# Optimization experiments

Hardware: AMD Instinct MI355X
Metric: run time of the kernel (lower is better)

## Reference

```python
import jax, jax.numpy as jnp
import numpy as np

# SLAYER neuron / simulation parameters (from netParams)
THETA = 10.0      # spike threshold
TAU_SR = 10.0     # synaptic (psp) alpha-kernel time constant
TAU_REF = 1.0     # refractory alpha-kernel time constant
SCALE_REF = 2.0   # refractory kernel scale
TS = 1.0          # simulation time step

N, C, H, W_SP, T = 8, 2, 50, 63, 500
OUT = 128


def _alpha_scan(x_t_first, tau, gain):
    """Causal convolution with alpha kernel k[dt] = gain*(dt*TS/tau)*exp(1-dt*TS/tau),
    k[0]=0, expressed as an exact 2-state linear recursion (O(T) instead of O(T^2)).
    x_t_first: [T, ...]. Returns [T, ...]."""
    r = jnp.exp(jnp.asarray(-TS / tau, x_t_first.dtype))
    c = jnp.asarray(gain * (TS / tau) * np.e, x_t_first.dtype)

    def step(carry, xt):
        A, B = carry          # A = sum c*dt*r^dt, B = sum c*r^dt over past inputs
        out = A               # kernel is 0 at dt=0, so x[t] does not contribute yet
        Bp = B + c * xt
        return (r * (A + Bp), r * Bp), out

    zeros = jnp.zeros_like(x_t_first[0])
    _, out = jax.lax.scan(step, (zeros, zeros), x_t_first)
    return out


def _spike_scan(u_t_first):
    """SLAYER getSpikes: sequential threshold with refractory alpha kernel
    nu[dt] = -SCALE_REF*THETA*(dt*TS/TAU_REF)*exp(1-dt*TS/TAU_REF).
    u_t_first: [T, N, O] membrane input. Returns spikes [T, N, O]."""
    r = jnp.exp(jnp.asarray(-TS / TAU_REF, u_t_first.dtype))
    c = jnp.asarray(-SCALE_REF * THETA * (TS / TAU_REF) * np.e, u_t_first.dtype)

    def step(carry, ut):
        A, B = carry
        u = ut + A                       # membrane + accumulated refractory response
        s = (u >= THETA).astype(u.dtype)
        Bp = B + c * s
        return (r * (A + Bp), r * Bp), s

    zeros = jnp.zeros_like(u_t_first[0])
    _, s = jax.lax.scan(step, (zeros, zeros), u_t_first)
    return s


def setup_inputs() -> dict:
    key = jax.random.key(0)
    k1, k2 = jax.random.split(key)
    downsampled = (jax.random.uniform(k1, (N, C, H, W_SP, T)) < 0.05).astype(jnp.float32)
    W = jax.random.normal(k2, (OUT, C * H * W_SP), dtype=jnp.float32) * 0.05
    return {"downsampled": downsampled, "W": W}


def reference(downsampled, W):
    # psp: alpha-kernel temporal filter over every input element
    x = jnp.moveaxis(downsampled, -1, 0)            # [T, N, C, H, W]
    a = _alpha_scan(x, TAU_SR, 1.0)                  # [T, N, C, H, W]
    # dense: full-spatial projection per time step
    a = a.reshape(T, N, C * H * W_SP)                # [T, N, CHW]
    u = jnp.einsum('tnc,oc->tno', a, W)              # [T, N, OUT]
    # spike generation with refractory dynamics
    s = _spike_scan(u)                               # [T, N, OUT]
    s = jnp.moveaxis(s, 0, -1)                       # [N, OUT, T]
    return s.reshape(N, OUT, 1, 1, T)                # SLAYER dense output layout
```

## Files before the change

kernel.cpp:

```cpp
#include <hip/hip_runtime.h>

#define NB 8
#define CHW 6300
#define TT 500
#define OUT 128
#define NO 1024
#define NK32 200
#define KSPLIT 8
#define NKC (NK32/KSPLIT)

typedef __attribute__((ext_vector_type(8))) _Float16 f16x8;
typedef __attribute__((ext_vector_type(4))) float f32x4;

__global__ __launch_bounds__(512) void packW(const float* __restrict__ W,
                                             _Float16* __restrict__ Wp) {
    const int tid = threadIdx.x;
    const int of = tid >> 6;
    const int lane = tid & 63;
    const int k32 = blockIdx.x;
    const int hl = blockIdx.y;
    const int o = of * 16 + (lane & 15);
    const int cb = k32 * 32 + (lane >> 4) * 8;

    union { _Float16 h[8]; uint4 u; } tmp;
#pragma unroll
    for (int i = 0; i < 8; i++) {
        int c = cb + i;
        float w = (c < CHW) ? W[(size_t)o * CHW + c] : 0.f;
        _Float16 hi = (_Float16)w;
        tmp.h[i] = (hl == 0) ? hi : (_Float16)((w - (float)hi) * 2048.f);
    }
    size_t lr = (((size_t)hl * NK32 + k32) * 8 + of) * 64 + lane;
    *(uint4*)(Wp + lr * 8) = tmp.u;
}

__global__ __launch_bounds__(256, 2) void gemm(const float* __restrict__ x,
                                               const _Float16* __restrict__ Wp,
                                               float* __restrict__ vp) {
    const int L = blockIdx.x;
    const int ks = L & 7;
    const int n  = (L >> 3) & 7;
    const int tg = L >> 6;
    const int tid = threadIdx.x;
    const int w = tid >> 6;
    const int lane = tid & 63;
    const int l15 = lane & 15;
    const int lg = lane >> 4;
    const int t0 = (tg * 4 + w) * 16;
    const int k32_0 = ks * NKC;

    __shared__ float Xl[4][32][17];

    const float* xn = x + (size_t)n * CHW * TT;
    const int xr = lane >> 2;
    const int xc4 = (lane & 3) * 4;
    const bool t_ok = (t0 + xc4 + 4) <= TT;
    const float4 f4z = make_float4(0.f, 0.f, 0.f, 0.f);

    f32x4 acc[8][2] = {};
    f16x8 wA[16], wB[16];
    float4 q0[2], q1[2];

#define XG(qq, it_)                                                            \
    {                                                                          \
        _Pragma("unroll") for (int p_ = 0; p_ < 2; p_++) {                     \
            const int c_ = (k32_0 + (it_)) * 32 + xr + 16 * p_;                \
            qq[p_] = (c_ < CHW && t_ok)                                        \
                ? *(const float4*)(xn + (size_t)c_ * TT + t0 + xc4)            \
                : f4z;                                                         \
        }                                                                      \
    }

#define DSW(qq)                                                                \
    {                                                                          \
        _Pragma("unroll") for (int p_ = 0; p_ < 2; p_++) {                     \
            const int r_ = xr + 16 * p_;                                       \
            Xl[w][r_][xc4 + 0] = qq[p_].x;                                     \
            Xl[w][r_][xc4 + 1] = qq[p_].y;                                     \
            Xl[w][r_][xc4 + 2] = qq[p_].z;                                     \
            Xl[w][r_][xc4 + 3] = qq[p_].w;                                     \
        }                                                                      \
    }

#define TRANS(bfr_)                                                            \
    {                                                                          \
        union { _Float16 h[8]; f16x8 v; } tc_;                                 \
        _Pragma("unroll") for (int i_ = 0; i_ < 8; i_++)                       \
            tc_.h[i_] = (_Float16)Xl[w][lg * 8 + i_][l15];                     \
        bfr_ = tc_.v;                                                          \
    }

#define WRL(wd, it_)                                                           \
    _Pragma("unroll") for (int f_ = 0; f_ < 16; f_++) {                        \
        const int hl_ = f_ & 1, of_ = f_ >> 1;                                 \
        wd[f_] = *(const f16x8*)(Wp +                                          \
            ((((size_t)hl_ * NK32 + k32_0 + (it_)) * 8 + of_) * 64 + lane) * 8); \
    }

#define COMP(bfr_, wd)                                                         \
    _Pragma("unroll") for (int of_ = 0; of_ < 8; of_++)                        \
        _Pragma("unroll") for (int hl_ = 0; hl_ < 2; hl_++)                    \
            acc[of_][hl_] = __builtin_amdgcn_mfma_f32_16x16x32_f16(            \
                wd[of_ * 2 + hl_], bfr_, acc[of_][hl_], 0, 0, 0);

    WRL(wA, 0)
    XG(q0, 0)
    XG(q1, 1)
    DSW(q0)

    for (int p = 0; p < 12; ++p) {
        {
            const int s = 2 * p;
            WRL(wB, s + 1)
            XG(q0, s + 2)
            f16x8 bfr;
            TRANS(bfr)
            DSW(q1)
            COMP(bfr, wA)
        }
        {
            const int s = 2 * p + 1;
            WRL(wA, s + 1)
            if (p < 11) { XG(q1, s + 2) }
            f16x8 bfr;
            TRANS(bfr)
            DSW(q0)
            COMP(bfr, wB)
        }
    }
    {
        f16x8 bfr;
        TRANS(bfr)
        COMP(bfr, wA)
    }

    const float inv = 1.f / 2048.f;
    const int t = t0 + l15;
    if (t < TT) {
#pragma unroll
        for (int of = 0; of < 8; of++) {
            f32x4 vo;
#pragma unroll
            for (int r = 0; r < 4; r++)
                vo[r] = acc[of][0][r] + acc[of][1][r] * inv;
            *(f32x4*)(vp + (((size_t)ks * TT + t) * NB + n) * OUT +
                      of * 16 + lg * 4) = vo;
        }
    }
#undef XG
#undef DSW
#undef TRANS
#undef WRL
#undef COMP
}

#define SCN_RA 0.9048374180359595f
#define SCN_RACA 0.24596031111569496f
#define SCN_RS 0.36787944117144233f
#define SCN_RSCS -20.0f
#define SCN_RSCS2 -40.0f
#define SCN_RSRSCS -7.3575888234288467f
#define SCN_TH 10.0f

#define CHAIN_STEP(i)                                                   \
    {                                                                   \
        float ua = Aa;                                                  \
        float w = fmaf(SCN_RS, G, ua);                                  \
        float u = sp ? (w + SCN_RSCS) : w;                              \
        bool sn = (u >= SCN_TH);                                        \
        sbuf[i][lane] = sn ? 1.f : 0.f;                                 \
        float Gb = fmaf(SCN_RS, G, H);                                  \
        G = sp ? (Gb + SCN_RSCS2) : Gb;                                 \
        float Hb = SCN_RS * H;                                          \
        H = sp ? (Hb + SCN_RSRSCS) : Hb;                                \
        sp = sn;                                                        \
        Ba = fmaf(SCN_RA, Ba, SCN_RACA * vv[i]);                        \
        Aa = fmaf(SCN_RA, Aa, Ba);                                      \
    }

__global__ __launch_bounds__(512) void scanspike(const float* __restrict__ vp,
                                                 float* __restrict__ out) {
    const int tid = threadIdx.x;
    const int wave = tid >> 6;
    const int lane = tid & 63;
    const int l5 = lane & 31;
    const int rh = lane >> 5;
    const int g0 = blockIdx.x * 32;
    const int cn = g0 >> 7;
    const int co = (g0 & 127) + l5;

    __shared__ float vbuf[2][64][32];
    __shared__ float sbuf[64][33];

    for (int rp = wave; rp * 2 < 64; rp += 8) {
        int r = rp * 2 + rh;
        float a = 0.f;
#pragma unroll
        for (int k = 0; k < KSPLIT; k++)
            a += vp[(((size_t)k * TT + r) * NB + cn) * OUT + co];
        vbuf[0][r][l5] = a;
    }
    __syncthreads();

    float Aa = 0.f, Ba = 0.f, G = 0.f, H = 0.f;
    bool sp = false;

    for (int tb = 0; tb < 8; ++tb) {
        const int cur = tb & 1;
        const int t0 = tb * 64;
        const int cnt = (tb == 7) ? 52 : 64;

        if (wave == 0) {
            if (lane < 32) {
                if (cnt == 64) {
                    float vv[64];
#pragma unroll
                    for (int i = 0; i < 64; ++i) vv[i] = vbuf[cur][i][l5];
#pragma unroll
                    for (int i = 0; i < 64; ++i) CHAIN_STEP(i)
                } else {
                    float vv[52];
#pragma unroll
                    for (int i = 0; i < 52; ++i) vv[i] = vbuf[cur][i][l5];
#pragma unroll
                    for (int i = 0; i < 52; ++i) CHAIN_STEP(i)
                }
            }
        } else if (tb < 7) {
            const int nt0 = t0 + 64;
            const int ncnt = (tb == 6) ? 52 : 64;
            for (int rp = wave - 1; rp * 2 < ncnt; rp += 7) {
                int r = rp * 2 + rh;
                float a = 0.f;
#pragma unroll
                for (int k = 0; k < KSPLIT; k++)
                    a += vp[(((size_t)k * TT + nt0 + r) * NB + cn) * OUT + co];
                vbuf[cur ^ 1][r][l5] = a;
            }
        }
        __syncthreads();

#pragma unroll
        for (int j = 0; j < 4; ++j) {
            int cc = wave * 4 + j;
            int oo = (g0 & 127) + cc;
            if (lane < cnt)
                out[((size_t)cn * OUT + oo) * TT + t0 + lane] = sbuf[lane][cc];
        }
        __syncthreads();
    }
}

extern "C" void kernel_launch(void* const* d_in, const int* in_sizes, int n_in,
                              void* d_out, int out_size, void* d_ws, size_t ws_size,
                              hipStream_t stream) {
    const float* x = (const float*)d_in[0];
    const float* W = (const float*)d_in[1];
    float* out = (float*)d_out;

    _Float16* Wp = (_Float16*)d_ws;
    float*    vp = (float*)((char*)d_ws + 3276800);

    packW<<<dim3(NK32, 2), 512, 0, stream>>>(W, Wp);
    gemm<<<512, 256, 0, stream>>>(x, Wp, vp);
    scanspike<<<32, 512, 0, stream>>>(vp, out);
}
```

Baseline: 72.63 us.

## Pre-stage activations to fp16 transposed layout and split GEMM waves over outputs

Adds an xstage kernel that converts the fp32 input to fp16 and writes it transposed into per-32-channel blocks, so the GEMM can load MFMA B-fragments directly with one 16-byte load instead of staging through LDS and converting. The GEMM now assigns waves to (time half, output half) tiles, doubles the grid to 1024 blocks and halves the accumulators and weight registers per wave. In exchange it adds a full extra read and write pass over the roughly 100 MB input (about 50 MB of fp16 written and read back) and another kernel launch.

```diff
diff --git a/kernel.cpp b/kernel.cpp
--- a/kernel.cpp
+++ b/kernel.cpp
@@ -34,124 +34,113 @@
     *(uint4*)(Wp + lr * 8) = tmp.u;
 }
 
-__global__ __launch_bounds__(256, 2) void gemm(const float* __restrict__ x,
+__global__ __launch_bounds__(256) void xstage(const float* __restrict__ x,
+                                              _Float16* __restrict__ xT2) {
+    const int k32 = blockIdx.x;
+    const int n   = blockIdx.y;
+    const int tid = threadIdx.x;
+    const int c0  = k32 * 32;
+    const int nc  = min(32, CHW - c0);
+
+    __shared__ _Float16 Xs[32][500];
+
+    if (nc < 32) {
+        for (int i = tid; i < 32 * 250; i += 256)
+            ((unsigned*)&Xs[0][0])[i] = 0u;
+        __syncthreads();
+    }
+    if (nc > 0) {
+        const float4* xr = (const float4*)(x + ((size_t)n * CHW + c0) * TT);
+        const int nf4 = nc * 125;
+        for (int i = tid; i < nf4; i += 256) {
+            float4 v = xr[i];
+            int cl = i / 125;
+            int tl = (i - cl * 125) * 4;
+            union { _Float16 h[4]; uint2 u; } pk;
+            pk.h[0] = (_Float16)v.x; pk.h[1] = (_Float16)v.y;
+            pk.h[2] = (_Float16)v.z; pk.h[3] = (_Float16)v.w;
+            *(uint2*)&Xs[cl][tl] = pk.u;
+        }
+    }
+    __syncthreads();
+
+    _Float16* op = xT2 + ((size_t)(n * NK32 + k32) * TT) * 32;
+    for (int t = tid; t < TT; t += 256) {
+        union { _Float16 h[32]; uint4 q[4]; } row;
+#pragma unroll
+        for (int c = 0; c < 32; ++c) row.h[c] = Xs[c][t];
+        uint4* dst = (uint4*)(op + (size_t)t * 32);
+        dst[0] = row.q[0]; dst[1] = row.q[1];
+        dst[2] = row.q[2]; dst[3] = row.q[3];
+    }
+}
+
+__global__ __launch_bounds__(256, 2) void gemm(const _Float16* __restrict__ xT2,
                                                const _Float16* __restrict__ Wp,
                                                float* __restrict__ vp) {
     const int L = blockIdx.x;
     const int ks = L & 7;
     const int n  = (L >> 3) & 7;
-    const int tg = L >> 6;
-    const int tid = threadIdx.x;
-    const int w = tid >> 6;
+    const int tt = L >> 6;
+    const int tid = threadIdx.x;
+    const int wave = tid >> 6;
     const int lane = tid & 63;
     const int l15 = lane & 15;
-    const int lg = lane >> 4;
-    const int t0 = (tg * 4 + w) * 16;
+    const int lg  = lane >> 4;
+    const int th = wave & 1;
+    const int oh = wave >> 1;
+    const int t0 = tt * 32 + th * 16;
     const int k32_0 = ks * NKC;
 
-    __shared__ float Xl[4][32][17];
-
-    const float* xn = x + (size_t)n * CHW * TT;
-    const int xr = lane >> 2;
-    const int xc4 = (lane & 3) * 4;
-    const bool t_ok = (t0 + xc4 + 4) <= TT;
-    const float4 f4z = make_float4(0.f, 0.f, 0.f, 0.f);
-
-    f32x4 acc[8][2] = {};
-    f16x8 wA[16], wB[16];
-    float4 q0[2], q1[2];
-
-#define XG(qq, it_)                                                            \
+    const _Float16* bbase = xT2 +
+        (((size_t)n * NK32 + k32_0) * TT + t0) * 32 + l15 * 32 + lg * 8;
+
+    f32x4 acc[4][2] = {};
+    f16x8 a0[8], a1[8];
+    uint4 b0, b1;
+
+#define BLD(bv, it_) bv = *(const uint4*)(bbase + (size_t)(it_) * (TT * 32));
+#define ALD(av, it_)                                                           \
+    _Pragma("unroll") for (int f_ = 0; f_ < 8; f_++) {                         \
+        const int hl_ = f_ & 1, of_ = f_ >> 1;                                 \
+        av[f_] = *(const f16x8*)(Wp +                                          \
+            ((((size_t)hl_ * NK32 + k32_0 + (it_)) * 8 + oh * 4 + of_) * 64 +  \
+             lane) * 8);                                                       \
+    }
+#define CMP(av, bv)                                                            \
     {                                                                          \
-        _Pragma("unroll") for (int p_ = 0; p_ < 2; p_++) {                     \
-            const int c_ = (k32_0 + (it_)) * 32 + xr + 16 * p_;                \
-            qq[p_] = (c_ < CHW && t_ok)                                        \
-                ? *(const float4*)(xn + (size_t)c_ * TT + t0 + xc4)            \
-                : f4z;                                                         \
-        }                                                                      \
-    }
-
-#define DSW(qq)                                                                \
-    {                                                                          \
-        _Pragma("unroll") for (int p_ = 0; p_ < 2; p_++) {                     \
-            const int r_ = xr + 16 * p_;                                       \
-            Xl[w][r_][xc4 + 0] = qq[p_].x;                                     \
-            Xl[w][r_][xc4 + 1] = qq[p_].y;                                     \
-            Xl[w][r_][xc4 + 2] = qq[p_].z;                                     \
-            Xl[w][r_][xc4 + 3] = qq[p_].w;                                     \
-        }                                                                      \
-    }
-
-#define TRANS(bfr_)                                                            \
-    {                                                                          \
-        union { _Float16 h[8]; f16x8 v; } tc_;                                 \
-        _Pragma("unroll") for (int i_ = 0; i_ < 8; i_++)                       \
-            tc_.h[i_] = (_Float16)Xl[w][lg * 8 + i_][l15];                     \
-        bfr_ = tc_.v;                                                          \
-    }
-
-#define WRL(wd, it_)                                                           \
-    _Pragma("unroll") for (int f_ = 0; f_ < 16; f_++) {                        \
-        const int hl_ = f_ & 1, of_ = f_ >> 1;                                 \
-        wd[f_] = *(const f16x8*)(Wp +                                          \
-            ((((size_t)hl_ * NK32 + k32_0 + (it_)) * 8 + of_) * 64 + lane) * 8); \
-    }
-
-#define COMP(bfr_, wd)                                                         \
-    _Pragma("unroll") for (int of_ = 0; of_ < 8; of_++)                        \
-        _Pragma("unroll") for (int hl_ = 0; hl_ < 2; hl_++)                    \
-            acc[of_][hl_] = __builtin_amdgcn_mfma_f32_16x16x32_f16(            \
-                wd[of_ * 2 + hl_], bfr_, acc[of_][hl_], 0, 0, 0);
-
-    WRL(wA, 0)
-    XG(q0, 0)
-    XG(q1, 1)
-    DSW(q0)
-
+        f16x8 bf = *(const f16x8*)&bv;                                         \
+        _Pragma("unroll") for (int of_ = 0; of_ < 4; of_++)                    \
+            _Pragma("unroll") for (int hl_ = 0; hl_ < 2; hl_++)                \
+                acc[of_][hl_] = __builtin_amdgcn_mfma_f32_16x16x32_f16(        \
+                    av[of_ * 2 + hl_], bf, acc[of_][hl_], 0, 0, 0);            \
+    }
+
+    ALD(a0, 0) BLD(b0, 0)
     for (int p = 0; p < 12; ++p) {
-        {
-            const int s = 2 * p;
-            WRL(wB, s + 1)
-            XG(q0, s + 2)
-            f16x8 bfr;
-            TRANS(bfr)
-            DSW(q1)
-            COMP(bfr, wA)
-        }
-        {
-            const int s = 2 * p + 1;
-            WRL(wA, s + 1)
-            if (p < 11) { XG(q1, s + 2) }
-            f16x8 bfr;
-            TRANS(bfr)
-            DSW(q0)
-            COMP(bfr, wB)
-        }
-    }
-    {
-        f16x8 bfr;
-        TRANS(bfr)
-        COMP(bfr, wA)
-    }
+        ALD(a1, 2 * p + 1) BLD(b1, 2 * p + 1)
+        CMP(a0, b0)
+        ALD(a0, 2 * p + 2) BLD(b0, 2 * p + 2)
+        CMP(a1, b1)
+    }
+    CMP(a0, b0)
 
     const float inv = 1.f / 2048.f;
     const int t = t0 + l15;
     if (t < TT) {
 #pragma unroll
-        for (int of = 0; of < 8; of++) {
+        for (int of = 0; of < 4; of++) {
             f32x4 vo;
 #pragma unroll
             for (int r = 0; r < 4; r++)
                 vo[r] = acc[of][0][r] + acc[of][1][r] * inv;
             *(f32x4*)(vp + (((size_t)ks * TT + t) * NB + n) * OUT +
-                      of * 16 + lg * 4) = vo;
-        }
-    }
-#undef XG
-#undef DSW
-#undef TRANS
-#undef WRL
-#undef COMP
+                      (oh * 4 + of) * 16 + lg * 4) = vo;
+        }
+    }
+#undef BLD
+#undef ALD
+#undef CMP
 }
 
 #define SCN_RA 0.9048374180359595f
@@ -258,10 +247,12 @@
     const float* W = (const float*)d_in[1];
     float* out = (float*)d_out;
 
-    _Float16* Wp = (_Float16*)d_ws;
-    float*    vp = (float*)((char*)d_ws + 3276800);
+    _Float16* Wp  = (_Float16*)d_ws;
+    _Float16* xT2 = (_Float16*)((char*)d_ws + 3276800);
+    float*    vp  = (float*)((char*)d_ws + 3276800 + 51204096);
 
     packW<<<dim3(NK32, 2), 512, 0, stream>>>(W, Wp);
-    gemm<<<512, 256, 0, stream>>>(x, Wp, vp);
+    xstage<<<dim3(NK32, NB), 256, 0, stream>>>(x, xT2);
+    gemm<<<1024, 256, 0, stream>>>(xT2, Wp, vp);
     scanspike<<<32, 512, 0, stream>>>(vp, out);
 }
```

Result: slower. 100.7 us (+38.7%).
